# Performance work log

Measured on AMD Instinct MI355X. Metric: run time of the kernel, lower is better.

The kernel has to match this reference:

```python
import jax, jax.numpy as jnp
from jax import lax
import numpy as np

A = 9            # anchors per location (3 scales x 3 ratios)
STRIDE = 16      # feat_stride
PRE_NMS = 6000   # top-k proposals before NMS (test mode)
POST_NMS = 300   # proposals kept after NMS (test mode)
NMS_T = 0.7      # NMS IoU threshold
MIN_SIZE = 16.0  # min proposal side length


def _anchor_ref(base=16, ratios=(0.5, 1.0, 2.0), scales=(8, 16, 32)):
    """Standard py-faster-rcnn anchor references, shape (9, 4)."""
    ratios = np.array(ratios, np.float64)
    scales = np.array(scales, np.float64)
    ctr = (base - 1) / 2.0
    size = float(base * base)
    ws = np.round(np.sqrt(size / ratios))
    hs = np.round(ws * ratios)
    ra = np.stack([ctr - 0.5 * (ws - 1), ctr - 0.5 * (hs - 1),
                   ctr + 0.5 * (ws - 1), ctr + 0.5 * (hs - 1)], 1)
    out = []
    for a in ra:
        w = a[2] - a[0] + 1.0
        h = a[3] - a[1] + 1.0
        cx = a[0] + 0.5 * (w - 1)
        cy = a[1] + 0.5 * (h - 1)
        ws2 = w * scales
        hs2 = h * scales
        out.append(np.stack([cx - 0.5 * (ws2 - 1), cy - 0.5 * (hs2 - 1),
                             cx + 0.5 * (ws2 - 1), cy + 0.5 * (hs2 - 1)], 1))
    return jnp.asarray(np.concatenate(out, 0), jnp.float32)


def _nms_keep(boxes):
    """Greedy NMS on score-sorted boxes (N,4) -> bool keep mask (N,)."""
    x1, y1, x2, y2 = boxes[:, 0], boxes[:, 1], boxes[:, 2], boxes[:, 3]
    areas = (x2 - x1 + 1.0) * (y2 - y1 + 1.0)
    iw = jnp.clip(jnp.minimum(x2[:, None], x2[None, :]) - jnp.maximum(x1[:, None], x1[None, :]) + 1.0, 0.0)
    ih = jnp.clip(jnp.minimum(y2[:, None], y2[None, :]) - jnp.maximum(y1[:, None], y1[None, :]) + 1.0, 0.0)
    inter = iw * ih
    iou = inter / (areas[:, None] + areas[None, :] - inter)
    n = boxes.shape[0]
    idx = jnp.arange(n)
    def body(i, keep):
        sup = (iou[i] > NMS_T) & (idx > i)
        return jnp.where(keep[i], keep & ~sup, keep)
    return lax.fori_loop(0, n, body, jnp.ones((n,), bool))


def _rpn_forward(feature_map, W_rpn, b_rpn, W_score, b_score, W_bbox, b_bbox, img_size):
    dn = ('NHWC', 'HWIO', 'NHWC')
    rpn = lax.conv_general_dilated(feature_map, W_rpn, (1, 1), 'SAME', dimension_numbers=dn) + b_rpn
    rpn = jax.nn.relu(rpn)
    cls = lax.conv_general_dilated(rpn, W_score, (1, 1), 'SAME', dimension_numbers=dn) + b_score
    bbx = lax.conv_general_dilated(rpn, W_bbox, (1, 1), 'SAME', dimension_numbers=dn) + b_bbox
    n, h, w, _ = feature_map.shape
    cls = cls.reshape(n, h, w, A, 2)
    prob = jax.nn.softmax(cls, axis=-1)
    fg = prob[..., 1].reshape(-1)           # (h*w*A,) foreground prob
    deltas = bbx.reshape(-1, 4)             # (h*w*A, 4)
    # anchors: shifts over (h, w), anchor-ref inner -> matches (h,w,A) flattening
    ref = _anchor_ref()
    sx = jnp.arange(w, dtype=jnp.float32) * STRIDE
    sy = jnp.arange(h, dtype=jnp.float32) * STRIDE
    ys, xs = jnp.meshgrid(sy, sx, indexing='ij')
    shifts = jnp.stack([xs, ys, xs, ys], -1).reshape(-1, 1, 4)
    anchors = (shifts + ref[None]).reshape(-1, 4)
    # decode deltas -> boxes
    aw = anchors[:, 2] - anchors[:, 0] + 1.0
    ah = anchors[:, 3] - anchors[:, 1] + 1.0
    acx = anchors[:, 0] + 0.5 * aw
    acy = anchors[:, 1] + 0.5 * ah
    pcx = deltas[:, 0] * aw + acx
    pcy = deltas[:, 1] * ah + acy
    pw = jnp.exp(deltas[:, 2]) * aw
    ph = jnp.exp(deltas[:, 3]) * ah
    imh = img_size[0].astype(jnp.float32)
    imw = img_size[1].astype(jnp.float32)
    boxes = jnp.stack([
        jnp.clip(pcx - 0.5 * pw, 0.0, imw - 1.0),
        jnp.clip(pcy - 0.5 * ph, 0.0, imh - 1.0),
        jnp.clip(pcx + 0.5 * pw, 0.0, imw - 1.0),
        jnp.clip(pcy + 0.5 * ph, 0.0, imh - 1.0)], -1)
    # min-size filter
    bw = boxes[:, 2] - boxes[:, 0] + 1.0
    bh = boxes[:, 3] - boxes[:, 1] + 1.0
    fg = jnp.where((bw >= MIN_SIZE) & (bh >= MIN_SIZE), fg, -1e9)
    # pre-NMS top-k (sorted descending)
    top_s, top_i = lax.top_k(fg, PRE_NMS)
    top_b = boxes[top_i]
    keep = _nms_keep(lax.stop_gradient(top_b))
    sel_s = jnp.where(keep, top_s, -1e9)
    _, sel_i = lax.top_k(sel_s, POST_NMS)
    rois = top_b[sel_i]
    ok = keep[sel_i] & (sel_s[sel_i] > -1e8)
    return jnp.where(ok[:, None], rois, 0.0)  # (POST_NMS, 4), zero-padded


def setup_inputs() -> dict:
    key = jax.random.key(0)
    ks = jax.random.split(key, 7)
    C_in, C_mid = 1024, 512
    std = 0.01
    return {
        'feature_map': jax.random.normal(ks[0], (1, 100, 150, C_in), jnp.float32),
        'W_rpn': jax.random.normal(ks[1], (3, 3, C_in, C_mid), jnp.float32) * std,
        'b_rpn': jnp.zeros((C_mid,), jnp.float32),
        'W_score': jax.random.normal(ks[2], (1, 1, C_mid, A * 2), jnp.float32) * std,
        'b_score': jnp.zeros((A * 2,), jnp.float32),
        'W_bbox': jax.random.normal(ks[3], (1, 1, C_mid, A * 4), jnp.float32) * std,
        'b_bbox': jnp.zeros((A * 4,), jnp.float32),
        'img_size': jnp.array([1600, 2400], jnp.int32),
    }


def reference(feature_map, W_rpn, b_rpn, W_score, b_score, W_bbox, b_bbox, img_size):
    return _rpn_forward(feature_map, W_rpn, b_rpn, W_score, b_score, W_bbox, b_bbox, img_size)
```

## Files before the change

kernel.cpp:

```cpp
#include <hip/hip_runtime.h>
#include <hip/hip_bf16.h>

typedef unsigned int u32;
typedef unsigned long long u64;

#define H_FM 100
#define W_FM 150
#define CIN 1024
#define CMID 512
#define NPIX 15000
#define NANCH 135000
#define PRE_NMS_N 6000
#define POST_NMS_N 300
#define WPR 94

#define PW 152
#define PH 104
#define PPIX (PW * PH)
#define CHSZ ((u64)PPIX * 64)
#define ASPLIT (32 * CHSZ)
#define BSPLIT ((u64)9216 * 512 * 2)

typedef __attribute__((ext_vector_type(8))) short short8;
typedef __attribute__((ext_vector_type(8))) __bf16 bf16x8;
typedef __attribute__((ext_vector_type(4))) float f32x4;

__device__ __forceinline__ u32 fkey(float f) {
  u32 u = __float_as_uint(f);
  return (u & 0x80000000u) ? ~u : (u | 0x80000000u);
}

__device__ __forceinline__ u64 shfl64(u64 v, int src) {
  u32 lo = (u32)__shfl((int)(u32)v, src, 64);
  u32 hi = (u32)__shfl((int)(u32)(v >> 32), src, 64);
  return ((u64)hi << 32) | (u64)lo;
}

struct FragArg {
  short8 v;
  __device__ operator short8() const { return v; }
  __device__ operator bf16x8() const { return __builtin_bit_cast(bf16x8, v); }
};
__device__ __forceinline__ f32x4 mfma16(short8 a, short8 b, f32x4 c) {
  return __builtin_amdgcn_mfma_f32_16x16x32_bf16(FragArg{a}, FragArg{b}, c, 0, 0, 0);
}

#define GLL(gp, lp) __builtin_amdgcn_global_load_lds(                        \
    (const __attribute__((address_space(1))) unsigned int*)(gp),             \
    (__attribute__((address_space(3))) unsigned int*)(lp), 16, 0, 0)

__device__ __forceinline__ void split3(float f, unsigned short& a,
                                       unsigned short& b, unsigned short& c) {
  __hip_bfloat16 h0 = __float2bfloat16(f);
  float f0 = __bfloat162float(h0);
  float r1 = f - f0;
  __hip_bfloat16 h1 = __float2bfloat16(r1);
  float r2 = r1 - __bfloat162float(h1);
  __hip_bfloat16 h2 = __float2bfloat16(r2);
  a = *(unsigned short*)&h0;
  b = *(unsigned short*)&h1;
  c = *(unsigned short*)&h2;
}

__global__ __launch_bounds__(256) void k_zeroA(unsigned short* __restrict__ Ap)
{
  int id = blockIdx.x * 256 + threadIdx.x;
  if (id >= 3 * 32 * 808) return;
  int sc = id / 808, h = id - sc * 808;
  int s = sc >> 5, c = sc & 31;
  int pp;
  if (h < 152) pp = h;
  else if (h < 608) pp = 101 * 152 + (h - 152);
  else { int k = h - 608; pp = ((k >> 1) + 1) * 152 + ((k & 1) ? 151 : 0); }
  float4* dst = (float4*)((char*)Ap + (u64)s * ASPLIT + (u64)c * CHSZ + (u64)pp * 64);
  float4 z = make_float4(0.f, 0.f, 0.f, 0.f);
  dst[0] = z; dst[1] = z; dst[2] = z; dst[3] = z;
}

__global__ __launch_bounds__(256) void k_splitA(
    const float* __restrict__ src, unsigned short* __restrict__ Ap)
{
  const int ntot = NPIX * 256;
  for (int id = blockIdx.x * 256 + threadIdx.x; id < ntot; id += gridDim.x * 256) {
    int p = id >> 8, g = id & 255;
    float4 v = *(const float4*)(src + (size_t)p * 1024 + g * 4);
    float f[4] = {v.x, v.y, v.z, v.w};
    ushort4 o0, o1, o2;
    unsigned short* q0 = (unsigned short*)&o0;
    unsigned short* q1 = (unsigned short*)&o1;
    unsigned short* q2 = (unsigned short*)&o2;
    #pragma unroll
    for (int e = 0; e < 4; ++e) split3(f[e], q0[e], q1[e], q2[e]);
    int yy = p / 150;
    int pp = (yy + 1) * 152 + (p - yy * 150) + 1;
    u64 off = (u64)(g >> 3) * CHSZ + (u64)pp * 64 + (g & 7) * 8;
    *(ushort4*)((char*)Ap + off) = o0;
    *(ushort4*)((char*)Ap + ASPLIT + off) = o1;
    *(ushort4*)((char*)Ap + 2 * ASPLIT + off) = o2;
  }
}

__global__ __launch_bounds__(256) void k_splitB(
    const float* __restrict__ Wsrc, unsigned short* __restrict__ Bp)
{
  __shared__ float tile[64][65];
  const int k0 = blockIdx.x * 64;
  const int n0 = blockIdx.y * 64;
  const int tid = threadIdx.x;
  const int lr = tid >> 4;
  const int lc = (tid & 15) * 4;
  #pragma unroll
  for (int rr = 0; rr < 64; rr += 16) {
    float4 v = *(const float4*)&Wsrc[(size_t)(k0 + lr + rr) * CMID + n0 + lc];
    tile[lr + rr][lc + 0] = v.x; tile[lr + rr][lc + 1] = v.y;
    tile[lr + rr][lc + 2] = v.z; tile[lr + rr][lc + 3] = v.w;
  }
  __syncthreads();
  const int n = n0 + (tid >> 2);
  const int kk = k0 + (tid & 3) * 16;
  unsigned short b0[16], b1[16], b2[16];
  #pragma unroll
  for (int e = 0; e < 16; ++e)
    split3(tile[(tid & 3) * 16 + e][tid >> 2], b0[e], b1[e], b2[e]);
  const int nblk = n >> 7, row = n & 127;
  const int seg = kk >> 10, chunk = (kk >> 5) & 31, ch = kk & 31;
  u64 base = ((u64)((nblk * 9 + seg) * 32 + chunk)) * 8192 + row * 64 + ch * 2;
  #pragma unroll
  for (int q = 0; q < 4; ++q) {
    *(ushort4*)((char*)Bp + base + q * 8) = *(ushort4*)&b0[q * 4];
    *(ushort4*)((char*)Bp + BSPLIT + base + q * 8) = *(ushort4*)&b1[q * 4];
    *(ushort4*)((char*)Bp + 2 * BSPLIT + base + q * 8) = *(ushort4*)&b2[q * 4];
  }
}

__global__ __launch_bounds__(256, 2) void k_conv8(
    const unsigned short* __restrict__ Ap, const unsigned short* __restrict__ Bp,
    const float* __restrict__ br, float* __restrict__ rpn)
{
  __shared__ char lds[49152];
  const int tid = threadIdx.x;
  const int L = tid & 63;
  const int w = tid >> 6;
  const int nblk = blockIdx.x & 3;
  const int bn = nblk * 128;
  const int bm = (blockIdx.x >> 2) * 128;
  const int wm = (w >> 1) * 64, wn = (w & 1) * 64;

  const int r = L >> 2;
  const u32 dqb = (u32)(((L & 3) ^ ((r >> 1) & 3)) * 16);

  int ay[2], ax[2];
  {
    int m0 = bm + w * 16 + r;       ay[0] = m0 / 150; ax[0] = m0 - ay[0] * 150;
    int m1 = bm + (w + 4) * 16 + r; ay[1] = m1 / 150; ax[1] = m1 - ay[1] * 150;
  }
  const u32 brow0 = (u32)((w * 16 + r) * 64) + dqb;
  const u32 brow1 = (u32)(((w + 4) * 16 + r) * 64) + dqb;
  const u64 bbase = (u64)nblk * 9 * 32 * 8192;

  const int fr = L & 15, fq = L >> 4;
  const u32 fsw = (u32)((fq ^ ((fr >> 1) & 3)) * 16);
  const u32 aF = (u32)((wm >> 4) * 1024 + fr * 64) + fsw;
  const u32 bF = 24576u + (u32)((wn >> 4) * 1024 + fr * 64) + fsw;

  u32 apix[2];
  auto segSetup = [&](int seg) {
    int dy = seg / 3 - 1, dx = seg - (seg / 3) * 3 - 1;
    apix[0] = (u32)(((ay[0] + dy + 1) * 152 + ax[0] + dx + 1) * 64) + dqb;
    apix[1] = (u32)(((ay[1] + dy + 1) * 152 + ax[1] + dx + 1) * 64) + dqb;
  };

  auto stage = [&](int seg, int chunk) {
    const u64 ach = (u64)chunk * CHSZ;
    #pragma unroll
    for (int s = 0; s < 3; ++s) {
      const char* as = (const char*)Ap + (u64)s * ASPLIT + ach;
      GLL(as + apix[0], lds + s * 8192 + w * 1024);
      GLL(as + apix[1], lds + s * 8192 + (w + 4) * 1024);
    }
    const u64 bch = bbase + (u64)(seg * 32 + chunk) * 8192;
    #pragma unroll
    for (int s = 0; s < 3; ++s) {
      const char* bs = (const char*)Bp + (u64)s * BSPLIT + bch;
      GLL(bs + brow0, lds + 24576 + s * 8192 + w * 1024);
      GLL(bs + brow1, lds + 24576 + s * 8192 + (w + 4) * 1024);
    }
  };

  short8 Af[3][4], Bf[3][4];
  auto readFrags = [&]() {
    #pragma unroll
    for (int s = 0; s < 3; ++s)
      #pragma unroll
      for (int i = 0; i < 4; ++i) {
        Af[s][i] = *(const short8*)(lds + aF + s * 8192 + i * 1024);
        Bf[s][i] = *(const short8*)(lds + bF + s * 8192 + i * 1024);
      }
  };

  f32x4 acc[4][4];
  #pragma unroll
  for (int i = 0; i < 4; ++i)
    #pragma unroll
    for (int j = 0; j < 4; ++j) acc[i][j] = (f32x4){0.f, 0.f, 0.f, 0.f};

  segSetup(0);
  stage(0, 0);
  __syncthreads();
  readFrags();

  for (int it = 0; it < 288; ++it) {
    const int nit = it + 1;
    const bool more = nit < 288;
    if (more && (nit & 31) == 0) segSetup(nit >> 5);
    __syncthreads();
    if (more) stage(nit >> 5, nit & 31);
    #pragma unroll
    for (int i = 0; i < 4; ++i)
      #pragma unroll
      for (int j = 0; j < 4; ++j) {
        f32x4 c = acc[i][j];
        c = mfma16(Af[0][i], Bf[0][j], c);
        c = mfma16(Af[0][i], Bf[1][j], c);
        c = mfma16(Af[1][i], Bf[0][j], c);
        c = mfma16(Af[1][i], Bf[1][j], c);
        c = mfma16(Af[0][i], Bf[2][j], c);
        c = mfma16(Af[2][i], Bf[0][j], c);
        acc[i][j] = c;
      }
    __syncthreads();
    if (more) readFrags();
  }

  #pragma unroll
  for (int i = 0; i < 4; ++i) {
    const int mb = bm + wm + i * 16 + ((L >> 4) << 2);
    #pragma unroll
    for (int ri = 0; ri < 4; ++ri) {
      const int m = mb + ri;
      if (m < NPIX) {
        float* op = rpn + (size_t)m * CMID;
        #pragma unroll
        for (int j = 0; j < 4; ++j) {
          const int n = bn + wn + j * 16 + (L & 15);
          op[n] = fmaxf(acc[i][j][ri] + br[n], 0.f);
        }
      }
    }
  }
}

__global__ __launch_bounds__(256) void k_packW(
    const float* __restrict__ Ws, const float* __restrict__ bs,
    const float* __restrict__ Wb, const float* __restrict__ bb,
    float* __restrict__ Wp, float* __restrict__ bp)
{
  int tt = blockIdx.x * 256 + threadIdx.x;
  int k = tt >> 6, o = tt & 63;
  float v = (o < 18) ? Ws[k * 18 + o] : ((o < 54) ? Wb[k * 36 + (o - 18)] : 0.f);
  Wp[tt] = v;
  if (tt < 64) bp[tt] = (tt < 18) ? bs[tt] : ((tt < 54) ? bb[tt - 18] : 0.f);
}

__global__ __launch_bounds__(256) void k_headgemm(
    const float* __restrict__ rpn, const float* __restrict__ Wp,
    const float* __restrict__ bp, float* __restrict__ vals)
{
  __shared__ float As[32][132];
  __shared__ float Bs[32][64];
  const int tid = threadIdx.x;
  const int bm = blockIdx.x * 128;
  const int mt = tid >> 3;
  const int nt = tid & 7;
  const int kg = tid & 7;
  const int ar = tid >> 3;
  const int n4 = (tid & 15) * 4;
  const int kr = tid >> 4;
  const float4 z4 = make_float4(0.f, 0.f, 0.f, 0.f);

  float acc[4][8];
  #pragma unroll
  for (int i = 0; i < 4; ++i)
    #pragma unroll
    for (int j = 0; j < 8; ++j) acc[i][j] = 0.f;

  for (int kc = 0; kc < 512; kc += 32) {
    __syncthreads();
    #pragma unroll
    for (int rr = 0; rr < 128; rr += 32) {
      int m = bm + ar + rr;
      float4 v = (m < NPIX) ? *(const float4*)&rpn[(size_t)m * CMID + kc + kg * 4] : z4;
      As[kg * 4 + 0][ar + rr] = v.x; As[kg * 4 + 1][ar + rr] = v.y;
      As[kg * 4 + 2][ar + rr] = v.z; As[kg * 4 + 3][ar + rr] = v.w;
    }
    *(float4*)&Bs[kr][n4]      = *(const float4*)&Wp[(kc + kr) * 64 + n4];
    *(float4*)&Bs[kr + 16][n4] = *(const float4*)&Wp[(kc + kr + 16) * 64 + n4];
    __syncthreads();
    #pragma unroll
    for (int kk = 0; kk < 32; ++kk) {
      float4 a = *(const float4*)&As[kk][mt * 4];
      float4 b0 = *(const float4*)&Bs[kk][nt * 8];
      float4 b1 = *(const float4*)&Bs[kk][nt * 8 + 4];
      float av[4] = {a.x, a.y, a.z, a.w};
      float bv[8] = {b0.x, b0.y, b0.z, b0.w, b1.x, b1.y, b1.z, b1.w};
      #pragma unroll
      for (int i = 0; i < 4; ++i)
        #pragma unroll
        for (int j = 0; j < 8; ++j) acc[i][j] = fmaf(av[i], bv[j], acc[i][j]);
    }
  }
  float bias[8];
  #pragma unroll
  for (int j = 0; j < 8; ++j) bias[j] = bp[nt * 8 + j];
  #pragma unroll
  for (int rI = 0; rI < 4; ++rI) {
    int m = bm + mt * 4 + rI;
    if (m < NPIX) {
      float o[8];
      #pragma unroll
      for (int j = 0; j < 8; ++j) o[j] = acc[rI][j] + bias[j];
      float* op = vals + (size_t)m * 64 + nt * 8;
      *(float4*)op = *(float4*)&o[0];
      *(float4*)(op + 4) = *(float4*)&o[4];
    }
  }
}

__global__ __launch_bounds__(256) void k_decode(
    const float* __restrict__ vals, const int* __restrict__ img,
    float* __restrict__ fg, float4* __restrict__ boxes)
{
  int gi = blockIdx.x * 256 + threadIdx.x;
  if (gi >= NANCH) return;
  const int p = gi / 9, a = gi - p * 9;
  const float AW[9] = {184.f, 368.f, 736.f, 128.f, 256.f, 512.f,  88.f, 176.f, 352.f};
  const float AH[9] = { 96.f, 192.f, 384.f, 128.f, 256.f, 512.f, 176.f, 352.f, 704.f};
  const int y = p / W_FM, x = p - y * W_FM;
  const float* row = vals + (size_t)p * 64;

  float c0 = row[2 * a], c1 = row[2 * a + 1];
  float score = 1.f / (1.f + expf(c0 - c1));

  float dxv = row[18 + 4 * a + 0];
  float dyv = row[18 + 4 * a + 1];
  float dwv = row[18 + 4 * a + 2];
  float dhv = row[18 + 4 * a + 3];

  float aw = AW[a], ah = AH[a];
  float acx = (float)(x * 16 + 8);
  float acy = (float)(y * 16 + 8);
  float pcx = dxv * aw + acx;
  float pcy = dyv * ah + acy;
  float pw = expf(dwv) * aw;
  float ph = expf(dhv) * ah;

  float imh1 = (float)img[0] - 1.f;
  float imw1 = (float)img[1] - 1.f;
  float b0 = fminf(fmaxf(pcx - 0.5f * pw, 0.f), imw1);
  float b1 = fminf(fmaxf(pcy - 0.5f * ph, 0.f), imh1);
  float b2 = fminf(fmaxf(pcx + 0.5f * pw, 0.f), imw1);
  float b3 = fminf(fmaxf(pcy + 0.5f * ph, 0.f), imh1);

  float bw = b2 - b0 + 1.f, bh = b3 - b1 + 1.f;
  if (!(bw >= 16.f && bh >= 16.f)) score = -1e9f;

  fg[gi] = score;
  boxes[gi] = make_float4(b0, b1, b2, b3);
}

__global__ void k_init(u32* __restrict__ hist, u32* __restrict__ ctl) {
  hist[threadIdx.x] = 0;
  if (threadIdx.x == 0) { ctl[0] = 0; ctl[1] = PRE_NMS_N; ctl[2] = 0; ctl[3] = 0; }
}

__global__ __launch_bounds__(256) void k_hist(
    const float* __restrict__ fg, u32* __restrict__ hist,
    const u32* __restrict__ ctl, int pass)
{
  __shared__ u32 h[256];
  h[threadIdx.x] = 0;
  __syncthreads();
  const int shift = 24 - 8 * pass;
  const u32 prefix = ctl[0];
  for (int i = blockIdx.x * 256 + threadIdx.x; i < NANCH; i += 128 * 256) {
    u32 key = fkey(fg[i]);
    bool match = (pass == 0) || ((key >> (shift + 8)) == prefix);
    if (match) atomicAdd(&h[(key >> shift) & 255], 1u);
  }
  __syncthreads();
  u32 c = h[threadIdx.x];
  if (c) atomicAdd(&hist[threadIdx.x], c);
}

__global__ void k_scan(u32* __restrict__ hist, u32* __restrict__ ctl) {
  if (threadIdx.x == 0) {
    u32 kneed = ctl[1];
    u32 cum = 0;
    int d = 0;
    for (int dd = 255; dd >= 0; --dd) {
      u32 c = hist[dd];
      if (cum + c >= kneed) { d = dd; break; }
      cum += c;
    }
    ctl[0] = (ctl[0] << 8) | (u32)d;
    ctl[1] = kneed - cum;
  }
  __syncthreads();
  hist[threadIdx.x] = 0;
}

__global__ __launch_bounds__(256) void k_compact(
    const float* __restrict__ fg, u32* __restrict__ ctl,
    u64* __restrict__ listA, u32* __restrict__ listB)
{
  int i = blockIdx.x * 256 + threadIdx.x;
  if (i >= NANCH) return;
  u32 T = ctl[0];
  u32 key = fkey(fg[i]);
  if (key > T) {
    u32 slot = atomicAdd(&ctl[2], 1u);
    listA[slot] = ((u64)key << 32) | (u64)(0xFFFFFFFFu - (u32)i);
  } else if (key == T) {
    u32 slot = atomicAdd(&ctl[3], 1u);
    if (slot < 8192) listB[slot] = (u32)i;
  }
}

__global__ __launch_bounds__(256) void k_tiefix(
    u32* __restrict__ ctl, const u32* __restrict__ listB, u64* __restrict__ listA)
{
  __shared__ u32 s[8192];
  const int tid = threadIdx.x;
  const u32 kneed = ctl[1];
  const u32 base = ctl[2];
  const u32 cntB = min(ctl[3], 8192u);
  const u32 T = ctl[0];
  if (kneed == 0) return;
  if (cntB == kneed) {
    for (u32 t = tid; t < kneed; t += 256)
      listA[base + t] = ((u64)T << 32) | (u64)(0xFFFFFFFFu - listB[t]);
    return;
  }
  u32 n2 = 1;
  while (n2 < cntB) n2 <<= 1;
  for (u32 i = tid; i < n2; i += 256) s[i] = (i < cntB) ? listB[i] : 0xFFFFFFFFu;
  __syncthreads();
  for (u32 k = 2; k <= n2; k <<= 1) {
    for (u32 j = k >> 1; j > 0; j >>= 1) {
      for (u32 i = tid; i < n2; i += 256) {
        u32 ixj = i ^ j;
        if (ixj > i) {
          u32 a = s[i], b = s[ixj];
          bool up = ((i & k) == 0);
          if ((a > b) == up) { s[i] = b; s[ixj] = a; }
        }
      }
      __syncthreads();
    }
  }
  for (u32 t = tid; t < kneed; t += 256)
    listA[base + t] = ((u64)T << 32) | (u64)(0xFFFFFFFFu - s[t]);
}

__global__ __launch_bounds__(1024) void k_sort(
    const u64* __restrict__ listA, u64* __restrict__ sorted)
{
  __shared__ u64 s[8192];
  const int tid = threadIdx.x;
  for (int i = tid; i < 8192; i += 1024) s[i] = (i < PRE_NMS_N) ? listA[i] : 0ull;
  __syncthreads();
  for (int k = 2; k <= 8192; k <<= 1) {
    for (int j = k >> 1; j > 0; j >>= 1) {
      for (int i = tid; i < 8192; i += 1024) {
        int ixj = i ^ j;
        if (ixj > i) {
          u64 a = s[i], b = s[ixj];
          bool up = ((i & k) == 0);
          if ((a < b) == up) { s[i] = b; s[ixj] = a; }
        }
      }
      __syncthreads();
    }
  }
  for (int i = tid; i < 8192; i += 1024) sorted[i] = s[i];
}

__global__ __launch_bounds__(256) void k_gather(
    const u64* __restrict__ sorted, const float4* __restrict__ boxes,
    float4* __restrict__ tb)
{
  int t = blockIdx.x * 256 + threadIdx.x;
  if (t >= PRE_NMS_N) return;
  u64 p = sorted[t];
  u32 idx = 0xFFFFFFFFu - (u32)(p & 0xFFFFFFFFull);
  tb[t] = boxes[idx];
}

__global__ __launch_bounds__(64) void k_mask(
    const float4* __restrict__ tb, u64* __restrict__ mask)
{
  __shared__ float4 cb[64];
  const int bj = blockIdx.x, bi = blockIdx.y, t = threadIdx.x;
  const int j0 = bj * 64;
  const int jn = min(64, PRE_NMS_N - j0);
  if (t < jn) cb[t] = tb[j0 + t];
  __syncthreads();
  const int i = bi * 64 + t;
  if (i >= PRE_NMS_N) return;
  const float4 b = tb[i];
  const float ai = (b.z - b.x + 1.f) * (b.w - b.y + 1.f);
  u64 bits = 0;
  for (int tt = 0; tt < jn; ++tt) {
    int j = j0 + tt;
    if (j <= i) continue;
    float4 c = cb[tt];
    float iw = fminf(b.z, c.z) - fmaxf(b.x, c.x) + 1.f;
    float ih = fminf(b.w, c.w) - fmaxf(b.y, c.y) + 1.f;
    float inter = fmaxf(iw, 0.f) * fmaxf(ih, 0.f);
    float aj = (c.z - c.x + 1.f) * (c.w - c.y + 1.f);
    float iou = inter / (ai + aj - inter);
    if (iou > 0.7f) bits |= (1ull << tt);
  }
  mask[(size_t)i * WPR + bj] = bits;
}

__global__ __launch_bounds__(64) void k_nms(
    const u64* __restrict__ mask, const float* __restrict__ tb,
    const u64* __restrict__ sorted, float* __restrict__ out)
{
  const int lane = threadIdx.x;
  u64 r0 = 0, r1 = 0;
  int kept = 0;
  const u32 kcut = fkey(-1e8f);
  for (int i = 0; i < PRE_NMS_N; ++i) {
    const int w = i >> 6, b = i & 63;
    u64 v0 = shfl64(r0, w & 63);
    u64 v1 = shfl64(r1, w & 63);
    u64 word = (w < 64) ? v0 : v1;
    if (!((word >> b) & 1ull)) {
      u32 key = (u32)(sorted[i] >> 32);
      if (key <= kcut) break;
      if (lane < 4) out[kept * 4 + lane] = tb[i * 4 + lane];
      ++kept;
      if (kept >= POST_NMS_N) break;
      const u64* row = mask + (size_t)i * WPR;
      r0 |= row[lane];
      if (lane < WPR - 64) r1 |= row[64 + lane];
    }
  }
  for (int j = kept * 4 + lane; j < POST_NMS_N * 4; j += 64) out[j] = 0.f;
}

extern "C" void kernel_launch(void* const* d_in, const int* in_sizes, int n_in,
                              void* d_out, int out_size, void* d_ws, size_t ws_size,
                              hipStream_t stream) {
  const float* fm  = (const float*)d_in[0];
  const float* Wr  = (const float*)d_in[1];
  const float* br  = (const float*)d_in[2];
  const float* Wsc = (const float*)d_in[3];
  const float* bsc = (const float*)d_in[4];
  const float* Wbb = (const float*)d_in[5];
  const float* bbb = (const float*)d_in[6];
  const int*   img = (const int*)d_in[7];
  float* out = (float*)d_out;

  char* w = (char*)d_ws;
  size_t off = 0;
  auto alloc = [&](size_t bytes) {
    size_t p = off;
    off = (off + bytes + 255) & ~(size_t)255;
    return p;
  };
  float* rpn    = (float*)(w + alloc((size_t)NPIX * CMID * 4));
  float* fg     = (float*)(w + alloc((size_t)NANCH * 4));
  float4* boxes = (float4*)(w + alloc((size_t)NANCH * 16));
  u32* hist     = (u32*)(w + alloc(1024));
  u32* ctl      = (u32*)(w + alloc(64));
  u64* listA    = (u64*)(w + alloc((size_t)PRE_NMS_N * 8));
  u32* listB    = (u32*)(w + alloc(8192 * 4));
  u64* sorted   = (u64*)(w + alloc(8192 * 8));
  float4* topbox= (float4*)(w + alloc((size_t)PRE_NMS_N * 16));
  u64* mask     = (u64*)(w + alloc((size_t)PRE_NMS_N * WPR * 8));
  float* Wp     = (float*)(w + alloc(512 * 64 * 4));
  float* bp     = (float*)(w + alloc(64 * 4));
  float* vals   = (float*)(w + alloc((size_t)NPIX * 64 * 4));
  unsigned short* Ap = (unsigned short*)(w + alloc((size_t)(3 * ASPLIT)));
  unsigned short* Bp = (unsigned short*)(w + alloc((size_t)(3 * BSPLIT)));

  k_zeroA<<<dim3((3 * 32 * 808 + 255) / 256), dim3(256), 0, stream>>>(Ap);
  k_splitA<<<dim3(1024), dim3(256), 0, stream>>>(fm, Ap);
  k_splitB<<<dim3(144, 8), dim3(256), 0, stream>>>(Wr, Bp);
  k_packW<<<dim3(128), dim3(256), 0, stream>>>(Wsc, bsc, Wbb, bbb, Wp, bp);
  k_conv8<<<dim3(118 * 4), dim3(256), 0, stream>>>(Ap, Bp, br, rpn);
  k_headgemm<<<dim3(118), dim3(256), 0, stream>>>(rpn, Wp, bp, vals);
  k_decode<<<dim3((NANCH + 255) / 256), dim3(256), 0, stream>>>(vals, img, fg, boxes);
  k_init<<<1, 256, 0, stream>>>(hist, ctl);
  for (int pass = 0; pass < 4; ++pass) {
    k_hist<<<128, 256, 0, stream>>>(fg, hist, ctl, pass);
    k_scan<<<1, 256, 0, stream>>>(hist, ctl);
  }
  k_compact<<<(NANCH + 255) / 256, 256, 0, stream>>>(fg, ctl, listA, listB);
  k_tiefix<<<1, 256, 0, stream>>>(ctl, listB, listA);
  k_sort<<<1, 1024, 0, stream>>>(listA, sorted);
  k_gather<<<(PRE_NMS_N + 255) / 256, 256, 0, stream>>>(sorted, boxes, topbox);
  k_mask<<<dim3(WPR, WPR), 64, 0, stream>>>(topbox, mask);
  k_nms<<<1, 64, 0, stream>>>(mask, (const float*)topbox, sorted, out);
}
```

Before: 1.238 ms.

## Fuse head GEMM with decode, merge init kernels, and skip suppressed NMS words

Folds zeroing of the padded A buffer into k_splitA and histogram/control init into k_packW, removing separate launches. Merges the 1x1 head GEMM and anchor decode into one kernel that keeps the 64 head outputs per pixel in shared memory, so the vals intermediate never goes through global memory. The new kernel uses smaller 32-row tiles across 472 blocks. NMS now walks only the live bits of each 64-bit word with ffs, bounded by a valid-count that k_gather computes with a ballot and atomic. This drops the per-index shuffle and the sorted-key read in the serial loop. The trade-off is lower per-thread reuse in the head GEMM.

New measurement: 1.176 ms. 5.0% less time.

```diff
diff --git a/kernel.cpp b/kernel.cpp
--- a/kernel.cpp
+++ b/kernel.cpp
@@ -62,24 +62,23 @@
   c = *(unsigned short*)&h2;
 }
 
-__global__ __launch_bounds__(256) void k_zeroA(unsigned short* __restrict__ Ap)
-{
-  int id = blockIdx.x * 256 + threadIdx.x;
-  if (id >= 3 * 32 * 808) return;
-  int sc = id / 808, h = id - sc * 808;
-  int s = sc >> 5, c = sc & 31;
-  int pp;
-  if (h < 152) pp = h;
-  else if (h < 608) pp = 101 * 152 + (h - 152);
-  else { int k = h - 608; pp = ((k >> 1) + 1) * 152 + ((k & 1) ? 151 : 0); }
-  float4* dst = (float4*)((char*)Ap + (u64)s * ASPLIT + (u64)c * CHSZ + (u64)pp * 64);
-  float4 z = make_float4(0.f, 0.f, 0.f, 0.f);
-  dst[0] = z; dst[1] = z; dst[2] = z; dst[3] = z;
-}
-
 __global__ __launch_bounds__(256) void k_splitA(
     const float* __restrict__ src, unsigned short* __restrict__ Ap)
 {
+  {
+    int z = blockIdx.x * 256 + threadIdx.x;
+    if (z < 3 * 32 * 808) {
+      int sc = z / 808, h = z - sc * 808;
+      int s = sc >> 5, c = sc & 31;
+      int pp;
+      if (h < 152) pp = h;
+      else if (h < 608) pp = 101 * 152 + (h - 152);
+      else { int k = h - 608; pp = ((k >> 1) + 1) * 152 + ((k & 1) ? 151 : 0); }
+      float4* dst = (float4*)((char*)Ap + (u64)s * ASPLIT + (u64)c * CHSZ + (u64)pp * 64);
+      float4 zz = make_float4(0.f, 0.f, 0.f, 0.f);
+      dst[0] = zz; dst[1] = zz; dst[2] = zz; dst[3] = zz;
+    }
+  }
   const int ntot = NPIX * 256;
   for (int id = blockIdx.x * 256 + threadIdx.x; id < ntot; id += gridDim.x * 256) {
     int p = id >> 8, g = id & 255;
@@ -253,124 +252,106 @@
 __global__ __launch_bounds__(256) void k_packW(
     const float* __restrict__ Ws, const float* __restrict__ bs,
     const float* __restrict__ Wb, const float* __restrict__ bb,
-    float* __restrict__ Wp, float* __restrict__ bp)
+    float* __restrict__ Wp, float* __restrict__ bp,
+    u32* __restrict__ hist, u32* __restrict__ ctl)
 {
   int tt = blockIdx.x * 256 + threadIdx.x;
   int k = tt >> 6, o = tt & 63;
   float v = (o < 18) ? Ws[k * 18 + o] : ((o < 54) ? Wb[k * 36 + (o - 18)] : 0.f);
   Wp[tt] = v;
   if (tt < 64) bp[tt] = (tt < 18) ? bs[tt] : ((tt < 54) ? bb[tt - 18] : 0.f);
-}
-
-__global__ __launch_bounds__(256) void k_headgemm(
+  if (tt < 256) hist[tt] = 0;
+  if (tt < 16) ctl[tt] = 0;
+  if (tt == 1) ctl[1] = PRE_NMS_N;
+}
+
+__global__ __launch_bounds__(256) void k_headdec(
     const float* __restrict__ rpn, const float* __restrict__ Wp,
-    const float* __restrict__ bp, float* __restrict__ vals)
-{
-  __shared__ float As[32][132];
+    const float* __restrict__ bp, const int* __restrict__ img,
+    float* __restrict__ fg, float4* __restrict__ boxes)
+{
+  __shared__ float As[32][33];
   __shared__ float Bs[32][64];
+  __shared__ float vs[32 * 64];
   const int tid = threadIdx.x;
-  const int bm = blockIdx.x * 128;
-  const int mt = tid >> 3;
-  const int nt = tid & 7;
+  const int bm = blockIdx.x * 32;
+  const int r  = tid >> 3;
   const int kg = tid & 7;
-  const int ar = tid >> 3;
+  const int c8 = (tid & 7) * 8;
   const int n4 = (tid & 15) * 4;
   const int kr = tid >> 4;
   const float4 z4 = make_float4(0.f, 0.f, 0.f, 0.f);
 
-  float acc[4][8];
-  #pragma unroll
-  for (int i = 0; i < 4; ++i)
-    #pragma unroll
-    for (int j = 0; j < 8; ++j) acc[i][j] = 0.f;
+  float acc[8];
+  #pragma unroll
+  for (int j = 0; j < 8; ++j) acc[j] = 0.f;
 
   for (int kc = 0; kc < 512; kc += 32) {
     __syncthreads();
-    #pragma unroll
-    for (int rr = 0; rr < 128; rr += 32) {
-      int m = bm + ar + rr;
+    {
+      int m = bm + r;
       float4 v = (m < NPIX) ? *(const float4*)&rpn[(size_t)m * CMID + kc + kg * 4] : z4;
-      As[kg * 4 + 0][ar + rr] = v.x; As[kg * 4 + 1][ar + rr] = v.y;
-      As[kg * 4 + 2][ar + rr] = v.z; As[kg * 4 + 3][ar + rr] = v.w;
+      As[kg * 4 + 0][r] = v.x; As[kg * 4 + 1][r] = v.y;
+      As[kg * 4 + 2][r] = v.z; As[kg * 4 + 3][r] = v.w;
     }
     *(float4*)&Bs[kr][n4]      = *(const float4*)&Wp[(kc + kr) * 64 + n4];
     *(float4*)&Bs[kr + 16][n4] = *(const float4*)&Wp[(kc + kr + 16) * 64 + n4];
     __syncthreads();
     #pragma unroll
     for (int kk = 0; kk < 32; ++kk) {
-      float4 a = *(const float4*)&As[kk][mt * 4];
-      float4 b0 = *(const float4*)&Bs[kk][nt * 8];
-      float4 b1 = *(const float4*)&Bs[kk][nt * 8 + 4];
-      float av[4] = {a.x, a.y, a.z, a.w};
-      float bv[8] = {b0.x, b0.y, b0.z, b0.w, b1.x, b1.y, b1.z, b1.w};
-      #pragma unroll
-      for (int i = 0; i < 4; ++i)
-        #pragma unroll
-        for (int j = 0; j < 8; ++j) acc[i][j] = fmaf(av[i], bv[j], acc[i][j]);
-    }
-  }
-  float bias[8];
-  #pragma unroll
-  for (int j = 0; j < 8; ++j) bias[j] = bp[nt * 8 + j];
-  #pragma unroll
-  for (int rI = 0; rI < 4; ++rI) {
-    int m = bm + mt * 4 + rI;
-    if (m < NPIX) {
-      float o[8];
-      #pragma unroll
-      for (int j = 0; j < 8; ++j) o[j] = acc[rI][j] + bias[j];
-      float* op = vals + (size_t)m * 64 + nt * 8;
-      *(float4*)op = *(float4*)&o[0];
-      *(float4*)(op + 4) = *(float4*)&o[4];
-    }
-  }
-}
-
-__global__ __launch_bounds__(256) void k_decode(
-    const float* __restrict__ vals, const int* __restrict__ img,
-    float* __restrict__ fg, float4* __restrict__ boxes)
-{
-  int gi = blockIdx.x * 256 + threadIdx.x;
-  if (gi >= NANCH) return;
-  const int p = gi / 9, a = gi - p * 9;
+      float a = As[kk][r];
+      float4 b0 = *(const float4*)&Bs[kk][c8];
+      float4 b1 = *(const float4*)&Bs[kk][c8 + 4];
+      acc[0] = fmaf(a, b0.x, acc[0]); acc[1] = fmaf(a, b0.y, acc[1]);
+      acc[2] = fmaf(a, b0.z, acc[2]); acc[3] = fmaf(a, b0.w, acc[3]);
+      acc[4] = fmaf(a, b1.x, acc[4]); acc[5] = fmaf(a, b1.y, acc[5]);
+      acc[6] = fmaf(a, b1.z, acc[6]); acc[7] = fmaf(a, b1.w, acc[7]);
+    }
+  }
+  __syncthreads();
+  #pragma unroll
+  for (int j = 0; j < 8; ++j) vs[r * 64 + c8 + j] = acc[j] + bp[c8 + j];
+  __syncthreads();
+
   const float AW[9] = {184.f, 368.f, 736.f, 128.f, 256.f, 512.f,  88.f, 176.f, 352.f};
   const float AH[9] = { 96.f, 192.f, 384.f, 128.f, 256.f, 512.f, 176.f, 352.f, 704.f};
-  const int y = p / W_FM, x = p - y * W_FM;
-  const float* row = vals + (size_t)p * 64;
-
-  float c0 = row[2 * a], c1 = row[2 * a + 1];
-  float score = 1.f / (1.f + expf(c0 - c1));
-
-  float dxv = row[18 + 4 * a + 0];
-  float dyv = row[18 + 4 * a + 1];
-  float dwv = row[18 + 4 * a + 2];
-  float dhv = row[18 + 4 * a + 3];
-
-  float aw = AW[a], ah = AH[a];
-  float acx = (float)(x * 16 + 8);
-  float acy = (float)(y * 16 + 8);
-  float pcx = dxv * aw + acx;
-  float pcy = dyv * ah + acy;
-  float pw = expf(dwv) * aw;
-  float ph = expf(dhv) * ah;
-
-  float imh1 = (float)img[0] - 1.f;
-  float imw1 = (float)img[1] - 1.f;
-  float b0 = fminf(fmaxf(pcx - 0.5f * pw, 0.f), imw1);
-  float b1 = fminf(fmaxf(pcy - 0.5f * ph, 0.f), imh1);
-  float b2 = fminf(fmaxf(pcx + 0.5f * pw, 0.f), imw1);
-  float b3 = fminf(fmaxf(pcy + 0.5f * ph, 0.f), imh1);
-
-  float bw = b2 - b0 + 1.f, bh = b3 - b1 + 1.f;
-  if (!(bw >= 16.f && bh >= 16.f)) score = -1e9f;
-
-  fg[gi] = score;
-  boxes[gi] = make_float4(b0, b1, b2, b3);
-}
-
-__global__ void k_init(u32* __restrict__ hist, u32* __restrict__ ctl) {
-  hist[threadIdx.x] = 0;
-  if (threadIdx.x == 0) { ctl[0] = 0; ctl[1] = PRE_NMS_N; ctl[2] = 0; ctl[3] = 0; }
+  const float imh1 = (float)img[0] - 1.f;
+  const float imw1 = (float)img[1] - 1.f;
+  for (int id = tid; id < 32 * 9; id += 256) {
+    int pl = id / 9, a = id - pl * 9;
+    int p = bm + pl;
+    if (p >= NPIX) break;
+    const float* row = vs + pl * 64;
+    const int y = p / W_FM, x = p - y * W_FM;
+
+    float c0 = row[2 * a], c1 = row[2 * a + 1];
+    float score = 1.f / (1.f + expf(c0 - c1));
+
+    float dxv = row[18 + 4 * a + 0];
+    float dyv = row[18 + 4 * a + 1];
+    float dwv = row[18 + 4 * a + 2];
+    float dhv = row[18 + 4 * a + 3];
+
+    float aw = AW[a], ah = AH[a];
+    float acx = (float)(x * 16 + 8);
+    float acy = (float)(y * 16 + 8);
+    float pcx = dxv * aw + acx;
+    float pcy = dyv * ah + acy;
+    float pw = expf(dwv) * aw;
+    float ph = expf(dhv) * ah;
+
+    float b0 = fminf(fmaxf(pcx - 0.5f * pw, 0.f), imw1);
+    float b1 = fminf(fmaxf(pcy - 0.5f * ph, 0.f), imh1);
+    float b2 = fminf(fmaxf(pcx + 0.5f * pw, 0.f), imw1);
+    float b3 = fminf(fmaxf(pcy + 0.5f * ph, 0.f), imh1);
+
+    float bw = b2 - b0 + 1.f, bh = b3 - b1 + 1.f;
+    if (!(bw >= 16.f && bh >= 16.f)) score = -1e9f;
+
+    int gi = p * 9 + a;
+    fg[gi] = score;
+    boxes[gi] = make_float4(b0, b1, b2, b3);
+  }
 }
 
 __global__ __launch_bounds__(256) void k_hist(
@@ -487,11 +468,16 @@
 
 __global__ __launch_bounds__(256) void k_gather(
     const u64* __restrict__ sorted, const float4* __restrict__ boxes,
-    float4* __restrict__ tb)
+    float4* __restrict__ tb, u32* __restrict__ ctl)
 {
   int t = blockIdx.x * 256 + threadIdx.x;
-  if (t >= PRE_NMS_N) return;
-  u64 p = sorted[t];
+  const u32 kcut = fkey(-1e8f);
+  bool inb = t < PRE_NMS_N;
+  u64 p = inb ? sorted[t] : 0ull;
+  bool valid = inb && ((u32)(p >> 32) > kcut);
+  u64 ball = __ballot(valid);
+  if ((threadIdx.x & 63) == 0 && ball) atomicAdd(&ctl[8], (u32)__popcll(ball));
+  if (!inb) return;
   u32 idx = 0xFFFFFFFFu - (u32)(p & 0xFFFFFFFFull);
   tb[t] = boxes[idx];
 }
@@ -526,26 +512,31 @@
 
 __global__ __launch_bounds__(64) void k_nms(
     const u64* __restrict__ mask, const float* __restrict__ tb,
-    const u64* __restrict__ sorted, float* __restrict__ out)
+    const u32* __restrict__ ctl, float* __restrict__ out)
 {
   const int lane = threadIdx.x;
+  const int nvalid = min((int)ctl[8], PRE_NMS_N);
   u64 r0 = 0, r1 = 0;
   int kept = 0;
-  const u32 kcut = fkey(-1e8f);
-  for (int i = 0; i < PRE_NMS_N; ++i) {
-    const int w = i >> 6, b = i & 63;
-    u64 v0 = shfl64(r0, w & 63);
-    u64 v1 = shfl64(r1, w & 63);
-    u64 word = (w < 64) ? v0 : v1;
-    if (!((word >> b) & 1ull)) {
-      u32 key = (u32)(sorted[i] >> 32);
-      if (key <= kcut) break;
+  for (int w = 0; w < WPR && kept < POST_NMS_N; ++w) {
+    const int base = w << 6;
+    if (base >= nvalid) break;
+    u64 rw = (w < 64) ? shfl64(r0, w) : shfl64(r1, w - 64);
+    u64 live = ~rw;
+    if (base + 64 > nvalid) live &= ((1ull << (nvalid - base)) - 1ull);
+    while (live) {
+      int b = (int)(__ffsll((long long)live) - 1);
+      int i = base + b;
       if (lane < 4) out[kept * 4 + lane] = tb[i * 4 + lane];
       ++kept;
       if (kept >= POST_NMS_N) break;
       const u64* row = mask + (size_t)i * WPR;
-      r0 |= row[lane];
-      if (lane < WPR - 64) r1 |= row[64 + lane];
+      u64 m0 = row[lane];
+      u64 m1 = (lane < WPR - 64) ? row[64 + lane] : 0ull;
+      r0 |= m0; r1 |= m1;
+      u64 rwi = (w < 64) ? shfl64(m0, w) : shfl64(m1, w - 64);
+      live &= ~rwi;
+      live = (b == 63) ? 0ull : (live & (~0ull << (b + 1)));
     }
   }
   for (int j = kept * 4 + lane; j < POST_NMS_N * 4; j += 64) out[j] = 0.f;
@@ -583,18 +574,14 @@
   u64* mask     = (u64*)(w + alloc((size_t)PRE_NMS_N * WPR * 8));
   float* Wp     = (float*)(w + alloc(512 * 64 * 4));
   float* bp     = (float*)(w + alloc(64 * 4));
-  float* vals   = (float*)(w + alloc((size_t)NPIX * 64 * 4));
   unsigned short* Ap = (unsigned short*)(w + alloc((size_t)(3 * ASPLIT)));
   unsigned short* Bp = (unsigned short*)(w + alloc((size_t)(3 * BSPLIT)));
 
-  k_zeroA<<<dim3((3 * 32 * 808 + 255) / 256), dim3(256), 0, stream>>>(Ap);
   k_splitA<<<dim3(1024), dim3(256), 0, stream>>>(fm, Ap);
   k_splitB<<<dim3(144, 8), dim3(256), 0, stream>>>(Wr, Bp);
-  k_packW<<<dim3(128), dim3(256), 0, stream>>>(Wsc, bsc, Wbb, bbb, Wp, bp);
+  k_packW<<<dim3(128), dim3(256), 0, stream>>>(Wsc, bsc, Wbb, bbb, Wp, bp, hist, ctl);
   k_conv8<<<dim3(118 * 4), dim3(256), 0, stream>>>(Ap, Bp, br, rpn);
-  k_headgemm<<<dim3(118), dim3(256), 0, stream>>>(rpn, Wp, bp, vals);
-  k_decode<<<dim3((NANCH + 255) / 256), dim3(256), 0, stream>>>(vals, img, fg, boxes);
-  k_init<<<1, 256, 0, stream>>>(hist, ctl);
+  k_headdec<<<dim3(472), dim3(256), 0, stream>>>(rpn, Wp, bp, img, fg, boxes);
   for (int pass = 0; pass < 4; ++pass) {
     k_hist<<<128, 256, 0, stream>>>(fg, hist, ctl, pass);
     k_scan<<<1, 256, 0, stream>>>(hist, ctl);
@@ -602,7 +589,7 @@
   k_compact<<<(NANCH + 255) / 256, 256, 0, stream>>>(fg, ctl, listA, listB);
   k_tiefix<<<1, 256, 0, stream>>>(ctl, listB, listA);
   k_sort<<<1, 1024, 0, stream>>>(listA, sorted);
-  k_gather<<<(PRE_NMS_N + 255) / 256, 256, 0, stream>>>(sorted, boxes, topbox);
+  k_gather<<<(PRE_NMS_N + 255) / 256, 256, 0, stream>>>(sorted, boxes, topbox, ctl);
   k_mask<<<dim3(WPR, WPR), 64, 0, stream>>>(topbox, mask);
-  k_nms<<<1, 64, 0, stream>>>(mask, (const float*)topbox, sorted, out);
-}
+  k_nms<<<1, 64, 0, stream>>>(mask, (const float*)topbox, ctl, out);
+}
```
